# Performance work log

Measured on AMD Instinct MI355X. Metric: run time of the kernel, lower is better.

## Reference

```python
import jax, jax.numpy as jnp
import numpy as np

N_WIRES = 10          # ceil(log2(32*32))
PIXELS = 1024         # 32*32 == 2**N_WIRES, so AmplitudeEmbedding needs no padding


def _rot_matrix(phi, theta, omega):
    # PennyLane Rot(phi, theta, omega) = RZ(omega) @ RY(theta) @ RZ(phi)
    c = jnp.cos(theta / 2).astype(jnp.complex64)
    s = jnp.sin(theta / 2).astype(jnp.complex64)
    e = lambda a: jnp.exp(1j * a.astype(jnp.complex64))
    m00 = e(-(phi + omega) / 2) * c
    m01 = -e((phi - omega) / 2) * s
    m10 = e((omega - phi) / 2) * s
    m11 = e((phi + omega) / 2) * c
    return jnp.stack([jnp.stack([m00, m01]), jnp.stack([m10, m11])])


def _apply_1q(state, U, wire):
    # state: (B, 2**N_WIRES) complex64; apply 2x2 U on `wire`
    s = state.reshape(-1, 2 ** wire, 2, 2 ** (N_WIRES - wire - 1))
    s = jnp.einsum('ij,bkjl->bkil', U, s)
    return s.reshape(-1, 2 ** N_WIRES)


def _apply_cnot(state, control, target):
    s = state.reshape((-1,) + (2,) * N_WIRES)
    s = jnp.moveaxis(s, (1 + control, 1 + target), (1, 2))
    # flip target amplitudes where control == 1
    s = jnp.stack([s[:, 0], s[:, 1, ::-1]], axis=1)
    s = jnp.moveaxis(s, (1, 2), (1 + control, 1 + target))
    return s.reshape(-1, 2 ** N_WIRES)


def _circuit(x_flat, weights):
    # AmplitudeEmbedding(normalize=True): 1024 features -> 2**10 amplitudes
    norm = jnp.linalg.norm(x_flat, axis=1, keepdims=True)
    state = (x_flat / norm).astype(jnp.complex64)
    # qw_map.tanh: squash raw params into bounded rotation angles
    angles = jnp.tanh(weights) * jnp.pi  # (qdepth, 10, 3)
    qdepth = weights.shape[0]
    for l in range(qdepth):
        for w in range(N_WIRES):
            U = _rot_matrix(angles[l, w, 0], angles[l, w, 1], angles[l, w, 2])
            state = _apply_1q(state, U, w)
        r = (l % (N_WIRES - 1)) + 1  # StronglyEntanglingLayers default ranges
        for w in range(N_WIRES):
            state = _apply_cnot(state, w, (w + r) % N_WIRES)
    return jnp.real(state * jnp.conj(state))  # probs, (B, 1024)


def setup_inputs() -> dict:
    key = jax.random.key(0)
    k1, k2 = jax.random.split(key)
    x = jax.random.normal(k1, (8192, 1, 32, 32), dtype=jnp.float32)
    weights = jax.random.normal(k2, (16, N_WIRES, 3), dtype=jnp.float32) * 0.4
    return {"x": x, "weights": weights}


def reference(x, weights):
    B = x.shape[0]
    x_flat = x.reshape(B, PIXELS)                 # 'b 1 w h -> b (w h)'
    probs = _circuit(x_flat, weights)             # (B, 1024)
    probs = probs[:, :PIXELS] * PIXELS            # rescale
    probs = jnp.clip(probs, 0.0, 1.0)
    return probs.reshape(B, 1, 32, 32)            # 'b (w h) -> b 1 w h'
```

## Files before the change

kernel.cpp:

```cpp
#include <hip/hip_runtime.h>
#include <math.h>

#define NW     10
#define DIM    1024
#define QDEPTH 16

typedef __attribute__((ext_vector_type(8))) _Float16 f16x8;
typedef __attribute__((ext_vector_type(4))) _Float16 f16x4;
typedef __attribute__((ext_vector_type(2))) _Float16 f16x2;
typedef __attribute__((ext_vector_type(4))) float    f32x4;

#define WS_GATES 0
#define WS_IPERM 8192
#define WS_INVS  81920
#define WS_XH    (1u << 20)
#define WS_BIL   (17u << 20)

#define SLOT(i) ((i) + ((i) >> 4))

__device__ inline void gate2(const float* __restrict__ g, float2& p0, float2& p1) {
    float m00r = g[0], m00i = g[1], m01r = g[2], m01i = g[3];
    float m10r = g[4], m10i = g[5], m11r = g[6], m11i = g[7];
    float n0x = m00r*p0.x - m00i*p0.y + m01r*p1.x - m01i*p1.y;
    float n0y = m00r*p0.y + m00i*p0.x + m01r*p1.y + m01i*p1.x;
    float n1x = m10r*p0.x - m10i*p0.y + m11r*p1.x - m11i*p1.y;
    float n1y = m10r*p0.y + m10i*p0.x + m11r*p1.y + m11i*p1.x;
    p0 = make_float2(n0x, n0y);
    p1 = make_float2(n1x, n1y);
}

__global__ __launch_bounds__(1024)
void prep_kernel(const float* __restrict__ w, float* __restrict__ gates,
                 int* __restrict__ iperm) {
    int t = threadIdx.x;
    const float PI = 3.14159265358979323846f;
    if (t < QDEPTH * NW) {
        float phi   = tanhf(w[t*3 + 0]) * PI;
        float theta = tanhf(w[t*3 + 1]) * PI;
        float omega = tanhf(w[t*3 + 2]) * PI;
        float ch = cosf(theta * 0.5f), sh = sinf(theta * 0.5f);
        float ap = (phi + omega) * 0.5f;
        float am = (phi - omega) * 0.5f;
        float* g = gates + t * 8;
        g[0] =  cosf(ap) * ch;  g[1] = -sinf(ap) * ch;
        g[2] = -cosf(am) * sh;  g[3] = -sinf(am) * sh;
        g[4] =  cosf(am) * sh;  g[5] = -sinf(am) * sh;
        g[6] =  cosf(ap) * ch;  g[7] =  sinf(ap) * ch;
    }
    int v = t;
    for (int l = 0; l < QDEPTH; ++l) {
        int r = (l % (NW - 1)) + 1;
        int u = v;
        for (int wq = NW - 1; wq >= 0; --wq) {
            int bc = 9 - wq;
            int bt = 9 - ((wq + r) % NW);
            u ^= ((u >> bc) & 1) << bt;
        }
        iperm[l * DIM + v] = u;
    }
}

__global__ __launch_bounds__(256)
void fused_sim_kernel(const float* __restrict__ gates, const int* __restrict__ iperm,
                      _Float16* __restrict__ Ucol,
                      const float* __restrict__ x, _Float16* __restrict__ Xh,
                      float* __restrict__ invs) {
    __shared__ float2 st[DIM + 64];
    const int bid = blockIdx.x;
    const int t   = threadIdx.x;

    if (bid >= 1024) {
        const int b = (bid - 1024) * 4 + (t >> 6);
        const int l = t & 63;
        const float4* xr = (const float4*)(x + (size_t)b * DIM);
        float4 v[4];
        float ss = 0.f;
        #pragma unroll
        for (int c = 0; c < 4; ++c) {
            v[c] = xr[l + c * 64];
            ss += v[c].x*v[c].x + v[c].y*v[c].y + v[c].z*v[c].z + v[c].w*v[c].w;
        }
        #pragma unroll
        for (int o = 32; o >= 1; o >>= 1) ss += __shfl_down(ss, o, 64);
        ss = __shfl(ss, 0, 64);
        if (l == 0) invs[b] = 1024.0f / ss;
        f16x4* xo = (f16x4*)(Xh + (size_t)b * DIM);
        #pragma unroll
        for (int c = 0; c < 4; ++c) {
            f16x4 h;
            h[0] = (_Float16)v[c].x; h[1] = (_Float16)v[c].y;
            h[2] = (_Float16)v[c].z; h[3] = (_Float16)v[c].w;
            xo[l + c * 64] = h;
        }
        return;
    }

    const int v = bid;

    int s4[4];
    #pragma unroll
    for (int k = 0; k < 4; ++k) s4[k] = SLOT(t + k * 256);
    int sq[4][4];
    #pragma unroll
    for (int pp = 0; pp < 4; ++pp) {
        const int b = 2 * pp;
        const int low = t & ((1 << b) - 1);
        const int i00 = ((t >> b) << (b + 2)) | low;
        sq[pp][0] = SLOT(i00);
        sq[pp][1] = SLOT(i00 | (1 << b));
        sq[pp][2] = SLOT(i00 | (2 << b));
        sq[pp][3] = SLOT(i00 | (3 << b));
    }

    #pragma unroll
    for (int k = 0; k < 4; ++k) {
        int i = t + k * 256;
        st[s4[k]] = make_float2(i == v ? 1.f : 0.f, 0.f);
    }
    __syncthreads();

    for (int l = 0; l < QDEPTH; ++l) {
        const float* gl = gates + l * NW * 8;

        float2 a00, a01, a10, a11;
        if (l == 0) {
            a00 = st[s4[0]]; a01 = st[s4[1]]; a10 = st[s4[2]]; a11 = st[s4[3]];
        } else {
            const int* ipm = iperm + (l - 1) * DIM;
            int g0 = ipm[t], g1 = ipm[t + 256], g2 = ipm[t + 512], g3 = ipm[t + 768];
            a00 = st[SLOT(g0)]; a01 = st[SLOT(g1)];
            a10 = st[SLOT(g2)]; a11 = st[SLOT(g3)];
        }
        gate2(gl + 0, a00, a10);
        gate2(gl + 0, a01, a11);
        gate2(gl + 8, a00, a01);
        gate2(gl + 8, a10, a11);
        if (l) __syncthreads();
        st[s4[0]] = a00; st[s4[1]] = a01; st[s4[2]] = a10; st[s4[3]] = a11;
        __syncthreads();

        #pragma unroll
        for (int pp = 3; pp >= 0; --pp) {
            const int b = 2 * pp;
            const float* gh = gl + (8 - b) * 8;
            const float* gm = gl + (9 - b) * 8;
            float2 c00 = st[sq[pp][0]], c01 = st[sq[pp][1]];
            float2 c10 = st[sq[pp][2]], c11 = st[sq[pp][3]];
            gate2(gh, c00, c10);
            gate2(gh, c01, c11);
            gate2(gm, c00, c01);
            gate2(gm, c10, c11);
            st[sq[pp][0]] = c00; st[sq[pp][1]] = c01;
            st[sq[pp][2]] = c10; st[sq[pp][3]] = c11;
            __syncthreads();
        }
    }

    const int* ipl = iperm + (QDEPTH - 1) * DIM;
    _Float16* col = Ucol + (size_t)v * 2048;
    #pragma unroll
    for (int k = 0; k < 4; ++k) {
        int i = t + k * 256;
        float2 a = st[SLOT(ipl[i])];
        f16x2 p;
        p[0] = (_Float16)a.x;
        p[1] = (_Float16)a.y;
        *(f16x2*)(col + 2 * i) = p;
    }
}

__global__ __launch_bounds__(256)
void transpose_kernel(const _Float16* __restrict__ Ucol, _Float16* __restrict__ Bil) {
    __shared__ _Float16 tile[64][72];
    const int bx = blockIdx.x;
    const int by = blockIdx.y;
    const int t  = threadIdx.x;
    const int r  = t >> 3;
    const int c8 = (t & 7) * 8;

    #pragma unroll
    for (int kk = 0; kk < 64; kk += 32) {
        *(f16x8*)&tile[kk + r][c8] =
            *(const f16x8*)(Ucol + (size_t)(by * 64 + kk + r) * 2048 + bx * 64 + c8);
    }
    __syncthreads();
    {
        f16x8 ore, oim;
        #pragma unroll
        for (int u = 0; u < 8; ++u) {
            ore[u] = tile[c8 + u][2 * r];
            oim[u] = tile[c8 + u][2 * r + 1];
        }
        const int j = bx * 32 + r;
        *(f16x8*)(Bil + (size_t)j * 1024 + by * 64 + c8) = ore;
        *(f16x8*)(Bil + (size_t)(1024 + j) * 1024 + by * 64 + c8) = oim;
    }
}

__device__ __forceinline__ f16x8 ldsfrag(const _Float16* base, int hrow, int c) {
    return *(const f16x8*)(base + hrow * 64 + ((c ^ (hrow & 7)) << 3));
}

#define NKT 16

__global__ __launch_bounds__(512, 2)
void gemm_kernel(const _Float16* __restrict__ A, const _Float16* __restrict__ B,
                 const float* __restrict__ invs, float* __restrict__ out) {
    __shared__ _Float16 As[2][2][8192];
    __shared__ _Float16 Bs[2][2][8192];
    const int t    = threadIdx.x;
    const int lane = t & 63;
    const int wid  = t >> 6;
    const int wm   = wid >> 2;
    const int wn   = wid & 3;

    const int bid   = blockIdx.x;
    const int local = bid >> 3;
    const int m0 = ((bid & 7) * 4 + (local & 3)) * 256;
    const int j0 = (local >> 2) * 128;

    const _Float16* Ag0 = A + (size_t)m0 * 1024;
    const _Float16* Ag1 = A + (size_t)(m0 + 128) * 1024;
    const _Float16* Bg0 = B + (size_t)j0 * 1024;
    const _Float16* Bg1 = B + (size_t)(1024 + j0) * 1024;

    const int srow = t >> 3;
    const int sgc  = ((t & 7) ^ (srow & 7)) * 8;
    #define STAGE_HALF(dst, gbase, kt)                                              \
        do {                                                                        \
            __builtin_amdgcn_global_load_lds(                                       \
                (const __attribute__((address_space(1))) void*)                     \
                    ((gbase) + (size_t)srow * 1024 + (kt) * 64 + sgc),              \
                (__attribute__((address_space(3))) void*)((dst) + t * 8), 16, 0, 0);\
            __builtin_amdgcn_global_load_lds(                                       \
                (const __attribute__((address_space(1))) void*)                     \
                    ((gbase) + (size_t)(64 + srow) * 1024 + (kt) * 64 + sgc),       \
                (__attribute__((address_space(3))) void*)((dst) + 4096 + t * 8),    \
                16, 0, 0);                                                          \
        } while (0)

    f32x4 acc[8][4];
    const f32x4 zero = {0.f, 0.f, 0.f, 0.f};
    #pragma unroll
    for (int i = 0; i < 8; ++i)
        #pragma unroll
        for (int j = 0; j < 4; ++j) acc[i][j] = zero;

    const int fr = lane & 15;
    const int ch = lane >> 4;
    const int brow = wn * 32;

    STAGE_HALF(&As[0][0][0], Ag0, 0);
    STAGE_HALF(&As[0][1][0], Ag1, 0);
    STAGE_HALF(&Bs[0][0][0], Bg0, 0);
    STAGE_HALF(&Bs[0][1][0], Bg1, 0);
    STAGE_HALF(&As[1][0][0], Ag0, 1);
    asm volatile("s_waitcnt vmcnt(2)" ::: "memory");
    __builtin_amdgcn_s_barrier();
    __builtin_amdgcn_sched_barrier(0);

    for (int tk = 0; tk < NKT; ++tk) {
        const int buf = tk & 1, nbuf = buf ^ 1;
        const _Float16* Ab   = &As[buf][wm][0];
        const _Float16* BbRe = &Bs[buf][0][0];
        const _Float16* BbIm = &Bs[buf][1][0];

        f16x8 afl[4][2], afh[4][2], bfa[2][2], bfb[2][2];

        #pragma unroll
        for (int m = 0; m < 4; ++m)
            #pragma unroll
            for (int ks = 0; ks < 2; ++ks)
                afl[m][ks] = ldsfrag(Ab, m * 16 + fr, ks * 4 + ch);
        #pragma unroll
        for (int n = 0; n < 2; ++n)
            #pragma unroll
            for (int ks = 0; ks < 2; ++ks)
                bfa[n][ks] = ldsfrag(BbRe, brow + n * 16 + fr, ks * 4 + ch);
        if (tk + 1 < NKT) STAGE_HALF(&As[nbuf][1][0], Ag1, tk + 1);
        __builtin_amdgcn_s_barrier();
        asm volatile("s_waitcnt lgkmcnt(0)" ::: "memory");
        __builtin_amdgcn_sched_barrier(0);
        __builtin_amdgcn_s_setprio(1);
        #pragma unroll
        for (int m = 0; m < 4; ++m)
            #pragma unroll
            for (int n = 0; n < 2; ++n)
                #pragma unroll
                for (int ks = 0; ks < 2; ++ks)
                    acc[m][n] = __builtin_amdgcn_mfma_f32_16x16x32_f16(
                        afl[m][ks], bfa[n][ks], acc[m][n], 0, 0, 0);
        __builtin_amdgcn_s_setprio(0);
        __builtin_amdgcn_s_barrier();
        __builtin_amdgcn_sched_barrier(0);

        #pragma unroll
        for (int n = 0; n < 2; ++n)
            #pragma unroll
            for (int ks = 0; ks < 2; ++ks)
                bfb[n][ks] = ldsfrag(BbIm, brow + n * 16 + fr, ks * 4 + ch);
        if (tk + 1 < NKT) STAGE_HALF(&Bs[nbuf][0][0], Bg0, tk + 1);
        __builtin_amdgcn_s_barrier();
        asm volatile("s_waitcnt lgkmcnt(0)" ::: "memory");
        __builtin_amdgcn_sched_barrier(0);
        __builtin_amdgcn_s_setprio(1);
        #pragma unroll
        for (int m = 0; m < 4; ++m)
            #pragma unroll
            for (int n = 0; n < 2; ++n)
                #pragma unroll
                for (int ks = 0; ks < 2; ++ks)
                    acc[m][2 + n] = __builtin_amdgcn_mfma_f32_16x16x32_f16(
                        afl[m][ks], bfb[n][ks], acc[m][2 + n], 0, 0, 0);
        __builtin_amdgcn_s_setprio(0);
        __builtin_amdgcn_s_barrier();
        __builtin_amdgcn_sched_barrier(0);

        #pragma unroll
        for (int m = 0; m < 4; ++m)
            #pragma unroll
            for (int ks = 0; ks < 2; ++ks)
                afh[m][ks] = ldsfrag(Ab, 64 + m * 16 + fr, ks * 4 + ch);
        if (tk + 1 < NKT) STAGE_HALF(&Bs[nbuf][1][0], Bg1, tk + 1);
        __builtin_amdgcn_s_barrier();
        asm volatile("s_waitcnt lgkmcnt(0)" ::: "memory");
        __builtin_amdgcn_sched_barrier(0);
        __builtin_amdgcn_s_setprio(1);
        #pragma unroll
        for (int m = 0; m < 4; ++m)
            #pragma unroll
            for (int n = 0; n < 2; ++n)
                #pragma unroll
                for (int ks = 0; ks < 2; ++ks)
                    acc[4 + m][n] = __builtin_amdgcn_mfma_f32_16x16x32_f16(
                        afh[m][ks], bfa[n][ks], acc[4 + m][n], 0, 0, 0);
        __builtin_amdgcn_s_setprio(0);
        __builtin_amdgcn_s_barrier();
        __builtin_amdgcn_sched_barrier(0);

        if (tk + 2 < NKT) STAGE_HALF(&As[buf][0][0], Ag0, tk + 2);
        __builtin_amdgcn_s_barrier();
        asm volatile("s_waitcnt lgkmcnt(0)" ::: "memory");
        __builtin_amdgcn_sched_barrier(0);
        __builtin_amdgcn_s_setprio(1);
        #pragma unroll
        for (int m = 0; m < 4; ++m)
            #pragma unroll
            for (int n = 0; n < 2; ++n)
                #pragma unroll
                for (int ks = 0; ks < 2; ++ks)
                    acc[4 + m][2 + n] = __builtin_amdgcn_mfma_f32_16x16x32_f16(
                        afh[m][ks], bfb[n][ks], acc[4 + m][2 + n], 0, 0, 0);
        __builtin_amdgcn_s_setprio(0);
        if (tk + 1 < NKT) {
            if (tk + 2 < NKT) asm volatile("s_waitcnt vmcnt(2)" ::: "memory");
            else              asm volatile("s_waitcnt vmcnt(0)" ::: "memory");
            __builtin_amdgcn_s_barrier();
            __builtin_amdgcn_sched_barrier(0);
        }
    }
    #undef STAGE_HALF

    const int colf = lane & 15;
    const int rowf = (lane >> 4) * 4;
    #pragma unroll
    for (int mf = 0; mf < 8; ++mf) {
        #pragma unroll
        for (int nf = 0; nf < 2; ++nf) {
            const int j = j0 + wn * 32 + nf * 16 + colf;
            #pragma unroll
            for (int r = 0; r < 4; ++r) {
                const int row = m0 + wm * 128 + mf * 16 + rowf + r;
                float re = acc[mf][nf][r];
                float im = acc[mf][2 + nf][r];
                float p = fminf((re * re + im * im) * invs[row], 1.0f);
                out[(size_t)row * DIM + j] = p;
            }
        }
    }
}

extern "C" void kernel_launch(void* const* d_in, const int* in_sizes, int n_in,
                              void* d_out, int out_size, void* d_ws, size_t ws_size,
                              hipStream_t stream) {
    const float* x = (const float*)d_in[0];
    const float* w = (const float*)d_in[1];
    float* out = (float*)d_out;

    char* ws = (char*)d_ws;
    float*     gates = (float*)(ws + WS_GATES);
    int*       iperm = (int*)(ws + WS_IPERM);
    float*     invs  = (float*)(ws + WS_INVS);
    _Float16*  Xh    = (_Float16*)(ws + WS_XH);
    _Float16*  Bil   = (_Float16*)(ws + WS_BIL);
    _Float16*  Ucol  = (_Float16*)d_out;

    prep_kernel<<<1, 1024, 0, stream>>>(w, gates, iperm);
    fused_sim_kernel<<<3072, 256, 0, stream>>>(gates, iperm, Ucol, x, Xh, invs);
    transpose_kernel<<<dim3(32, 16), 256, 0, stream>>>(Ucol, Bil);
    gemm_kernel<<<256, 512, 0, stream>>>(Xh, Bil, invs, out);
}
```

Measured before the change: 113.8 us.

## Drop block barriers in wave-local gate stages and prefetch permutation indices

Result: no change. 112.2 us (-1.4%).

```diff
diff --git a/kernel.cpp b/kernel.cpp
--- a/kernel.cpp
+++ b/kernel.cpp
@@ -119,17 +119,23 @@
     }
     __syncthreads();
 
+    int pg0 = 0, pg1 = 0, pg2 = 0, pg3 = 0;
+
     for (int l = 0; l < QDEPTH; ++l) {
         const float* gl = gates + l * NW * 8;
+
+        if (l) __syncthreads();
 
         float2 a00, a01, a10, a11;
         if (l == 0) {
             a00 = st[s4[0]]; a01 = st[s4[1]]; a10 = st[s4[2]]; a11 = st[s4[3]];
         } else {
-            const int* ipm = iperm + (l - 1) * DIM;
-            int g0 = ipm[t], g1 = ipm[t + 256], g2 = ipm[t + 512], g3 = ipm[t + 768];
-            a00 = st[SLOT(g0)]; a01 = st[SLOT(g1)];
-            a10 = st[SLOT(g2)]; a11 = st[SLOT(g3)];
+            a00 = st[SLOT(pg0)]; a01 = st[SLOT(pg1)];
+            a10 = st[SLOT(pg2)]; a11 = st[SLOT(pg3)];
+        }
+        {
+            const int* ipn = iperm + l * DIM;
+            pg0 = ipn[t]; pg1 = ipn[t + 256]; pg2 = ipn[t + 512]; pg3 = ipn[t + 768];
         }
         gate2(gl + 0, a00, a10);
         gate2(gl + 0, a01, a11);
@@ -152,20 +158,25 @@
             gate2(gm, c10, c11);
             st[sq[pp][0]] = c00; st[sq[pp][1]] = c01;
             st[sq[pp][2]] = c10; st[sq[pp][3]] = c11;
-            __syncthreads();
-        }
-    }
-
-    const int* ipl = iperm + (QDEPTH - 1) * DIM;
+            asm volatile("s_waitcnt lgkmcnt(0)" ::: "memory");
+            __builtin_amdgcn_sched_barrier(0);
+        }
+    }
+
+    __syncthreads();
     _Float16* col = Ucol + (size_t)v * 2048;
-    #pragma unroll
-    for (int k = 0; k < 4; ++k) {
-        int i = t + k * 256;
-        float2 a = st[SLOT(ipl[i])];
-        f16x2 p;
-        p[0] = (_Float16)a.x;
-        p[1] = (_Float16)a.y;
-        *(f16x2*)(col + 2 * i) = p;
+    {
+        float2 a0 = st[SLOT(pg0)], a1 = st[SLOT(pg1)];
+        float2 a2 = st[SLOT(pg2)], a3 = st[SLOT(pg3)];
+        f16x2 p0, p1, p2, p3;
+        p0[0] = (_Float16)a0.x; p0[1] = (_Float16)a0.y;
+        p1[0] = (_Float16)a1.x; p1[1] = (_Float16)a1.y;
+        p2[0] = (_Float16)a2.x; p2[1] = (_Float16)a2.y;
+        p3[0] = (_Float16)a3.x; p3[1] = (_Float16)a3.y;
+        *(f16x2*)(col + 2 * t)         = p0;
+        *(f16x2*)(col + 2 * (t + 256)) = p1;
+        *(f16x2*)(col + 2 * (t + 512)) = p2;
+        *(f16x2*)(col + 2 * (t + 768)) = p3;
     }
 }
 
```
